# Kernel tuning notes

Measured on AMD Instinct MI355X. Metric: run time of the kernel, lower is better.

The kernel has to match this reference:

```python
import jax, jax.numpy as jnp
import numpy as np

B, L, D, H, DK, DV = 16, 1024, 512, 8, 64, 64
FACTOR = 1
TOP_K = int(FACTOR * np.log(L))  # 6, static


def autocorrelation(q, k, v, top_k):
    # q, k, v: [B, L, H, E] (Autoformer layout)
    Bs, Ls, Hs, Es = q.shape
    qp = jnp.transpose(q, (0, 2, 3, 1))  # [B,H,E,L]
    kp = jnp.transpose(k, (0, 2, 3, 1))
    vp = jnp.transpose(v, (0, 2, 3, 1))
    qf = jnp.fft.rfft(qp, axis=-1)
    kf = jnp.fft.rfft(kp, axis=-1)
    corr = jnp.fft.irfft(qf * jnp.conj(kf), n=Ls, axis=-1)  # [B,H,E,L]
    # time_delay_agg_training: average corr over heads and channels
    mean_value = corr.mean(axis=(1, 2))  # [B,L]
    _, index = jax.lax.top_k(mean_value.mean(axis=0), top_k)  # [top_k] shared delays
    weights = jnp.take(mean_value, index, axis=1)  # [B,top_k]
    tmp_corr = jax.nn.softmax(weights, axis=-1)  # [B,top_k]
    # roll(v, -delay) gathered for all top_k delays at once
    idx = (index[:, None] + jnp.arange(Ls)[None, :]) % Ls  # [top_k, L]
    patterns = vp[..., idx]  # [B,H,E,top_k,L]
    agg = jnp.einsum('bhekl,bk->bhel', patterns, tmp_corr)  # [B,H,E,L]
    return jnp.transpose(agg, (0, 3, 1, 2))  # [B,L,H,E]


def setup_inputs() -> dict:
    key = jax.random.key(0)
    ks = jax.random.split(key, 7)
    Q = jax.random.normal(ks[0], (B, L, D), jnp.float32)
    K = jax.random.normal(ks[1], (B, L, D), jnp.float32)
    V = jax.random.normal(ks[2], (B, L, D), jnp.float32)
    attn_mask = jnp.zeros((B, 1, L, L), jnp.bool_)  # ignored by AutoCorrelation
    s = 0.02
    WQ = jax.random.normal(ks[3], (D, H * DK), jnp.float32) * s
    WK = jax.random.normal(ks[4], (D, H * DK), jnp.float32) * s
    WV = jax.random.normal(ks[5], (D, H * DV), jnp.float32) * s
    Wfc = jax.random.normal(ks[6], (H * DV, D), jnp.float32) * s
    return {"Q": Q, "K": K, "V": V, "attn_mask": attn_mask,
            "WQ": WQ, "WK": WK, "WV": WV, "Wfc": Wfc}


def reference(Q, K, V, attn_mask, WQ, WK, WV, Wfc):
    del attn_mask  # full AutoCorrelation ignores the mask
    q_s = (Q @ WQ).reshape(B, L, H, DK)  # [B,L,H,dk]
    k_s = (K @ WK).reshape(B, L, H, DK)
    v_s = (V @ WV).reshape(B, L, H, DV)
    out = autocorrelation(q_s, k_s, v_s, TOP_K)  # [B,L,H,dv]
    context = out.reshape(B, L, H * DV)
    return context @ Wfc  # [B,L,D]
```

## Files before the change

kernel.cpp:

```cpp
#include <hip/hip_runtime.h>
#include <math.h>

namespace {

constexpr int Bb = 16;
constexpr int Ll = 1024;
constexpr int Dd = 512;
constexpr int TOPK = 6;
constexpr int Kc = 512;

typedef short  short8 __attribute__((ext_vector_type(8)));
typedef float  f32x4  __attribute__((ext_vector_type(4)));

__device__ __forceinline__ short f2bf(float x) {
  unsigned u = __builtin_bit_cast(unsigned, x);
  u += 0x7fffu + ((u >> 16) & 1u);
  return (short)(u >> 16);
}
__device__ __forceinline__ float bf2f(short b) {
  unsigned u = ((unsigned)(unsigned short)b) << 16;
  return __builtin_bit_cast(float, u);
}
__device__ __forceinline__ void g2l16(const void* g, void* l) {
  __builtin_amdgcn_global_load_lds(
      (const __attribute__((address_space(1))) unsigned*)g,
      (__attribute__((address_space(3))) unsigned*)l, 16, 0, 0);
}
__device__ __forceinline__ short8 cvt8(float4 a, float4 b) {
  short8 o;
  o[0] = f2bf(a.x); o[1] = f2bf(a.y); o[2] = f2bf(a.z); o[3] = f2bf(a.w);
  o[4] = f2bf(b.x); o[5] = f2bf(b.y); o[6] = f2bf(b.z); o[7] = f2bf(b.w);
  return o;
}

#define BARRIER() do { asm volatile("" ::: "memory"); \
    __builtin_amdgcn_s_barrier(); \
    asm volatile("" ::: "memory"); } while (0)
#define VMCNT8() asm volatile("s_waitcnt vmcnt(8)" ::: "memory")
#define VMCNT4() asm volatile("s_waitcnt vmcnt(4)" ::: "memory")
#define VMCNT0() asm volatile("s_waitcnt vmcnt(0)" ::: "memory")
#define LGKM0()  do { asm volatile("s_waitcnt lgkmcnt(0)" ::: "memory"); \
    __builtin_amdgcn_sched_barrier(0); } while (0)

template<int MODE>
__global__ __launch_bounds__(256) void g64(
    const void* __restrict__ A0, const void* __restrict__ A1,
    const short* __restrict__ B0, const short* __restrict__ B1,
    void* __restrict__ C0, void* __restrict__ C1)
{
  __shared__ short lds[2][16384];
  __shared__ float bins[256];

  const int tid = threadIdx.x;
  int z, m0, n0;
  if (MODE == 0) {
    z = blockIdx.x >> 4;
    const int s = blockIdx.x & 15;
    m0 = (s >> 2) * 128;  n0 = (s & 3) * 128;
  } else if (MODE == 1) {
    z = blockIdx.z;
    const int fb = blockIdx.x;
    const int s  = (fb & 7) * 64 + (fb >> 3);
    m0 = (s >> 2) * 128;  n0 = (s & 3) * 128;
  } else {
    const int fb = blockIdx.x;
    const int s  = (fb & 7) * 128 + (fb >> 3);
    z  = s >> 6;
    m0 = ((s >> 3) & 7) * 128;  n0 = (s & 7) * 128;
  }

  const int rS  = tid >> 3;
  const int c8S = (tid & 7) ^ (rS & 7);
  const short* Ga = nullptr;  const float* Fa = nullptr;
  const short* Gb = nullptr;  const float* Fb = nullptr;
  if (MODE == 0) {
    Ga = (const short*)(z ? A1 : A0) + (size_t)(m0 + rS) * Kc + c8S * 8;
    Gb = (z ? B1 : B0) + (size_t)(n0 + rS) * Kc + c8S * 8;
  } else if (MODE == 1) {
    Fa = (const float*)(z ? A1 : A0) + (size_t)(m0 + rS) * Kc + c8S * 8;
    Gb = (z ? B1 : B0) + (size_t)(n0 + rS) * Kc + c8S * 8;
  } else {
    Ga = (const short*)A0 + (size_t)z * Ll * Kc + (size_t)(m0 + rS) * Kc + c8S * 8;
    Fb = (const float*)A1 + (size_t)z * Ll * Kc + (size_t)(n0 + rS) * Kc + c8S * 8;
  }

  const int lane = tid & 63;
  const int wid  = tid >> 6;
  const int wr = wid >> 1, wn = wid & 1;
  const int lo = lane & 15, hi = lane >> 4;
  int aoff[2][4], boff[2][4];
#pragma unroll
  for (int i = 0; i < 4; ++i) {
    const int ar = wr * 64 + i * 16 + lo;
    const int br = wn * 64 + i * 16 + lo;
#pragma unroll
    for (int ks = 0; ks < 2; ++ks) {
      aoff[ks][i] = (ar * 8 + ((ks * 4 + hi) ^ (ar & 7))) * 8;
      boff[ks][i] = 8192 + (br * 8 + ((ks * 4 + hi) ^ (br & 7))) * 8;
    }
  }

  if (MODE == 2) bins[tid] = 0.f;

  f32x4 acc[4][4];
#pragma unroll
  for (int i = 0; i < 4; ++i)
#pragma unroll
    for (int j = 0; j < 4; ++j) acc[i][j] = (f32x4){0.f, 0.f, 0.f, 0.f};

#define SG_A(buf, kt) do { _Pragma("unroll") \
    for (int i_ = 0; i_ < 4; ++i_) \
      g2l16(Ga + (size_t)i_ * 32 * Kc + (kt) * 64, &lds[buf][(i_ * 256 + tid) * 8]); } while (0)
#define SG_B(buf, kt) do { _Pragma("unroll") \
    for (int i_ = 0; i_ < 4; ++i_) \
      g2l16(Gb + (size_t)i_ * 32 * Kc + (kt) * 64, &lds[buf][8192 + (i_ * 256 + tid) * 8]); } while (0)
#define LD_F(eV, F, kt) do { _Pragma("unroll") \
    for (int i_ = 0; i_ < 4; ++i_) { \
      eV[2 * i_]     = *(const float4*)((F) + (size_t)i_ * 32 * Kc + (kt) * 64); \
      eV[2 * i_ + 1] = *(const float4*)((F) + (size_t)i_ * 32 * Kc + (kt) * 64 + 4); } } while (0)
#define WR_F(buf, opb, eV) do { _Pragma("unroll") \
    for (int i_ = 0; i_ < 4; ++i_) \
      *(short8*)&lds[buf][(opb) + (i_ * 256 + tid) * 8] = cvt8(eV[2 * i_], eV[2 * i_ + 1]); } while (0)

  {
    float4 e[8];
    if (MODE == 1) {
      SG_B(0, 0); LD_F(e, Fa, 0); WR_F(0, 0, e);
      SG_B(1, 1); LD_F(e, Fa, 1); WR_F(1, 0, e);
    } else if (MODE == 2) {
      SG_A(0, 0); LD_F(e, Fb, 0); WR_F(0, 8192, e);
      SG_A(1, 1); LD_F(e, Fb, 1); WR_F(1, 8192, e);
    } else {
      SG_A(0, 0); SG_B(0, 0);
      SG_A(1, 1); SG_B(1, 1);
    }
  }

  int cur = 0;
#pragma unroll 1
  for (int t = 0; t < 8; ++t) {
    if (t == 7)            VMCNT0();
    else if (MODE == 0)    VMCNT8();
    else                   VMCNT4();
    LGKM0();
    BARRIER();

    const short* L = lds[cur];
    const bool pf = (t < 6);
    float4 e[8];

    short8 af[4], bq[4];
#pragma unroll
    for (int i = 0; i < 4; ++i) af[i] = *(const short8*)(L + aoff[0][i]);
#pragma unroll
    for (int j = 0; j < 4; ++j) bq[j] = *(const short8*)(L + boff[0][j]);
    if (pf && MODE == 1) LD_F(e, Fa, t + 2);
    if (pf && MODE == 2) LD_F(e, Fb, t + 2);
#pragma unroll
    for (int i = 0; i < 4; ++i)
#pragma unroll
      for (int j = 0; j < 4; ++j)
        acc[i][j] = __builtin_amdgcn_mfma_f32_16x16x32_bf16(af[i], bq[j], acc[i][j], 0, 0, 0);
#pragma unroll
    for (int i = 0; i < 4; ++i) af[i] = *(const short8*)(L + aoff[1][i]);
#pragma unroll
    for (int j = 0; j < 4; ++j) bq[j] = *(const short8*)(L + boff[1][j]);
#pragma unroll
    for (int i = 0; i < 4; ++i)
#pragma unroll
      for (int j = 0; j < 4; ++j)
        acc[i][j] = __builtin_amdgcn_mfma_f32_16x16x32_bf16(af[i], bq[j], acc[i][j], 0, 0, 0);

    BARRIER();

    if (pf) {
      if (MODE == 1)      { SG_B(cur, t + 2); WR_F(cur, 0, e); }
      else if (MODE == 2) { SG_A(cur, t + 2); WR_F(cur, 8192, e); }
      else                { SG_A(cur, t + 2); SG_B(cur, t + 2); }
    }
    cur ^= 1;
  }
#undef SG_A
#undef SG_B
#undef LD_F
#undef WR_F

  if (MODE != 2) {
    short* C = (short*)(MODE == 0 ? (z ? C1 : C0) : (z ? C1 : C0));
#pragma unroll
    for (int i = 0; i < 4; ++i)
#pragma unroll
      for (int r = 0; r < 4; ++r) {
        const size_t row = m0 + wr * 64 + i * 16 + hi * 4 + r;
#pragma unroll
        for (int j = 0; j < 4; ++j)
          C[row * Dd + n0 + wn * 64 + j * 16 + lo] = f2bf(acc[i][j][r]);
      }
  } else {
    float red[7][4];
#pragma unroll
    for (int d = 0; d < 7; ++d)
#pragma unroll
      for (int r = 0; r < 4; ++r) red[d][r] = 0.f;
#pragma unroll
    for (int i = 0; i < 4; ++i)
#pragma unroll
      for (int j = 0; j < 4; ++j)
#pragma unroll
        for (int r = 0; r < 4; ++r) red[i - j + 3][r] += acc[i][j][r];

    const int dbase = 127 + (wr - wn) * 64 + 4 * hi - lo;
#pragma unroll
    for (int d = 0; d < 7; ++d)
#pragma unroll
      for (int r = 0; r < 4; ++r)
        atomicAdd(&bins[dbase + 16 * (d - 3) + r], red[d][r]);
    __syncthreads();
    if (tid < 255) {
      float* mv = (float*)C0;
      const int l = (m0 - n0 + tid - 127) & (Ll - 1);
      atomicAdd(&mv[z * Ll + l], bins[tid]);
    }
  }
}

__global__ __launch_bounds__(256) void prep(
    const float* __restrict__ WQ, const float* __restrict__ WK,
    const float* __restrict__ WV, const float* __restrict__ Wfc,
    short* __restrict__ wqb, short* __restrict__ wkb,
    short* __restrict__ wvb, short* __restrict__ wtf,
    float* __restrict__ mv)
{
  const int z = blockIdx.z;
  const int tx = threadIdx.x & 31, ty = threadIdx.x >> 5;
  const int bx = blockIdx.x, by = blockIdx.y;
  if (z < 3) {
    const float* W = (z == 0) ? WQ : (z == 1) ? WK : WV;
    short* O = (z == 0) ? wqb : (z == 1) ? wkb : wvb;
#pragma unroll
    for (int s = 0; s < 32; s += 8) {
      const size_t o = (size_t)(by * 32 + ty + s) * 512 + bx * 32 + tx;
      O[o] = f2bf(W[o]);
    }
    if (z == 0 && threadIdx.x < 64) {
      const int fb = by * 16 + bx;
      mv[fb * 64 + threadIdx.x] = 0.f;
    }
  } else {
    __shared__ float t[32][33];
#pragma unroll
    for (int s = 0; s < 32; s += 8)
      t[ty + s][tx] = Wfc[(size_t)(by * 32 + ty + s) * 512 + bx * 32 + tx];
    __syncthreads();
#pragma unroll
    for (int s = 0; s < 32; s += 8)
      wtf[(size_t)(bx * 32 + ty + s) * 512 + by * 32 + tx] = f2bf(t[tx][ty + s]);
  }
}

__global__ __launch_bounds__(1024) void topk_softmax(
    const float* __restrict__ mean_value,
    int* __restrict__ idx_out, float* __restrict__ w_out)
{
  __shared__ float vals[1024];
  __shared__ int   inds[1024];
  __shared__ float bm[1024];
  __shared__ int   topi[TOPK];
  const int t = threadIdx.x;
  float s = 0.f;
  for (int b = 0; b < Bb; ++b) s += mean_value[b * Ll + t];
  bm[t] = s;
  __syncthreads();
  for (int k = 0; k < TOPK; ++k) {
    bool taken = false;
    for (int j = 0; j < k; ++j) taken |= (topi[j] == t);
    vals[t] = taken ? -INFINITY : bm[t];
    inds[t] = t;
    __syncthreads();
    for (int stride = 512; stride > 0; stride >>= 1) {
      if (t < stride) {
        if (vals[t + stride] > vals[t]) { vals[t] = vals[t + stride]; inds[t] = inds[t + stride]; }
      }
      __syncthreads();
    }
    if (t == 0) topi[k] = inds[0];
    __syncthreads();
  }
  if (t < TOPK) idx_out[t] = topi[t];
  if (t < Bb) {
    float wv[TOPK], mx = -INFINITY;
#pragma unroll
    for (int k = 0; k < TOPK; ++k) {
      wv[k] = mean_value[t * Ll + topi[k]] * (1.f / 512.f);
      mx = fmaxf(mx, wv[k]);
    }
    float sum = 0.f;
#pragma unroll
    for (int k = 0; k < TOPK; ++k) { wv[k] = expf(wv[k] - mx); sum += wv[k]; }
#pragma unroll
    for (int k = 0; k < TOPK; ++k) w_out[t * TOPK + k] = wv[k] / sum;
  }
}

__global__ __launch_bounds__(256) void gather_out(
    const short* __restrict__ U, const float* __restrict__ w,
    const int* __restrict__ idx, float* __restrict__ out)
{
  const int b = blockIdx.y;
  __shared__ float ww[8];
  __shared__ int   ii[8];
  if (threadIdx.x < TOPK) { ww[threadIdx.x] = w[b * TOPK + threadIdx.x]; ii[threadIdx.x] = idx[threadIdx.x]; }
  __syncthreads();
  const int l = blockIdx.x * 4 + (threadIdx.x >> 6);
  const int c = (threadIdx.x & 63) * 8;
  const short* ub = U + (size_t)b * Ll * Dd;
  float a[8] = {};
#pragma unroll
  for (int k = 0; k < TOPK; ++k) {
    const short8 vv = *(const short8*)&ub[(size_t)((l + ii[k]) & (Ll - 1)) * Dd + c];
    const float wk = ww[k];
#pragma unroll
    for (int e = 0; e < 8; ++e) a[e] = fmaf(wk, bf2f(vv[e]), a[e]);
  }
  float* op = &out[((size_t)b * Ll + l) * Dd + c];
  *(float4*)op       = make_float4(a[0], a[1], a[2], a[3]);
  *(float4*)(op + 4) = make_float4(a[4], a[5], a[6], a[7]);
}

}

extern "C" void kernel_launch(void* const* d_in, const int* in_sizes, int n_in,
                              void* d_out, int out_size, void* d_ws, size_t ws_size,
                              hipStream_t stream)
{
  const float* Q   = (const float*)d_in[0];
  const float* K   = (const float*)d_in[1];
  const float* V   = (const float*)d_in[2];
  const float* WQ  = (const float*)d_in[4];
  const float* WK  = (const float*)d_in[5];
  const float* WV  = (const float*)d_in[6];
  const float* Wfc = (const float*)d_in[7];
  float* out = (float*)d_out;

  char* ws = (char*)d_ws;
  const size_t SB = (size_t)Bb * Ll * Dd * sizeof(short);
  short* T    = (short*)(ws);
  short* U    = (short*)(ws + 1 * SB);
  short* wqb  = (short*)(ws + 2 * SB);
  short* wkb  = wqb + 512 * 512;
  short* wvb  = wkb + 512 * 512;
  short* wtf  = wvb + 512 * 512;
  short* Gt   = wtf + 512 * 512;
  short* Ht   = Gt  + 512 * 512;
  float* mv   = (float*)(Ht + 512 * 512);
  float* w    = mv + Bb * Ll;
  int*   idx  = (int*)(w + 128);

  prep<<<dim3(16, 16, 4), 256, 0, stream>>>(WQ, WK, WV, Wfc, wqb, wkb, wvb, wtf, mv);

  g64<0><<<32, 256, 0, stream>>>(wkb, wtf, wqb, wvb, Gt, Ht);

  g64<1><<<dim3(512, 1, 2), 256, 0, stream>>>(Q, V, Gt, Ht, T, U);

  g64<2><<<1024, 256, 0, stream>>>(T, K, nullptr, nullptr, mv, nullptr);

  topk_softmax<<<1, 1024, 0, stream>>>(mv, idx, w);

  gather_out<<<dim3(Ll / 4, Bb), 256, 0, stream>>>(U, w, idx, out);
}
```

Measured before the change: 138.4 us.

## Rewrite GEMM kernels with smaller tiles, split-K correlation, and fused K conversion

Replaces the 128x128, K-step-64 GEMM template with 128x64 tiles and K-step 32, reads fp32 operands directly with in-register bf16 conversion, and sets launch_bounds occupancy to 4. The K-to-bf16 conversion moves into extra blocks of the mode-1 launch, and the correlation GEMM is split along K into two halves with more blocks that accumulate through atomics. The WK and Wfc bf16 preconversions are dropped, and a new grid remapping is applied. The aim is more blocks in flight and better latency hiding, at the cost of more barriers, more atomics and less data reuse per tile.

```diff
diff --git a/kernel.cpp b/kernel.cpp
--- a/kernel.cpp
+++ b/kernel.cpp
@@ -7,7 +7,6 @@
 constexpr int Ll = 1024;
 constexpr int Dd = 512;
 constexpr int TOPK = 6;
-constexpr int Kc = 512;
 
 typedef short  short8 __attribute__((ext_vector_type(8)));
 typedef float  f32x4  __attribute__((ext_vector_type(4)));
@@ -33,210 +32,212 @@
   return o;
 }
 
-#define BARRIER() do { asm volatile("" ::: "memory"); \
-    __builtin_amdgcn_s_barrier(); \
-    asm volatile("" ::: "memory"); } while (0)
-#define VMCNT8() asm volatile("s_waitcnt vmcnt(8)" ::: "memory")
-#define VMCNT4() asm volatile("s_waitcnt vmcnt(4)" ::: "memory")
-#define VMCNT0() asm volatile("s_waitcnt vmcnt(0)" ::: "memory")
-#define LGKM0()  do { asm volatile("s_waitcnt lgkmcnt(0)" ::: "memory"); \
-    __builtin_amdgcn_sched_barrier(0); } while (0)
-
 template<int MODE>
-__global__ __launch_bounds__(256) void g64(
+__global__ __launch_bounds__(256, 4) void gk(
     const void* __restrict__ A0, const void* __restrict__ A1,
     const short* __restrict__ B0, const short* __restrict__ B1,
-    void* __restrict__ C0, void* __restrict__ C1)
-{
-  __shared__ short lds[2][16384];
-  __shared__ float bins[256];
+    void* __restrict__ C0, void* __restrict__ C1,
+    const float* __restrict__ KfIn, short* __restrict__ kbOut)
+{
+  __shared__ short lds[(MODE == 2) ? 12288 : 8192];
+  __shared__ float bins[(MODE == 2) ? 192 : 1];
 
   const int tid = threadIdx.x;
-  int z, m0, n0;
+  int z = 0, m0 = 0, n0 = 0, koff = 0;
+  const float* Fa = nullptr;
+  const short* Ab = nullptr;
+  const short* Bp = nullptr;
+
   if (MODE == 0) {
-    z = blockIdx.x >> 4;
-    const int s = blockIdx.x & 15;
-    m0 = (s >> 2) * 128;  n0 = (s & 3) * 128;
+    const int fb = blockIdx.x;
+    z  = fb >> 5;
+    m0 = ((fb >> 3) & 3) * 128;
+    n0 = (fb & 7) * 64;
+    Fa = (const float*)(z ? A1 : A0);
+    Bp = z ? B1 : B0;
   } else if (MODE == 1) {
-    z = blockIdx.z;
     const int fb = blockIdx.x;
-    const int s  = (fb & 7) * 64 + (fb >> 3);
-    m0 = (s >> 2) * 128;  n0 = (s & 3) * 128;
+    const int s  = (fb & 7) * 288 + (fb >> 3);
+    if (s >= 2048) {
+      const int ci = s - 2048;
+#pragma unroll
+      for (int it = 0; it < 16; ++it) {
+        const size_t i8 = (size_t)(ci * 256 + tid) + (size_t)it * 65536;
+        const float4 a = *(const float4*)(KfIn + i8 * 8);
+        const float4 b = *(const float4*)(KfIn + i8 * 8 + 4);
+        *(short8*)&kbOut[i8 * 8] = cvt8(a, b);
+      }
+      return;
+    }
+    z  = s >> 10;
+    const int ss = s & 1023;
+    m0 = (ss >> 3) * 128;
+    n0 = (ss & 7) * 64;
+    Fa = (const float*)(z ? A1 : A0);
+    Bp = z ? B1 : B0;
   } else {
     const int fb = blockIdx.x;
-    const int s  = (fb & 7) * 128 + (fb >> 3);
-    z  = s >> 6;
-    m0 = ((s >> 3) & 7) * 128;  n0 = (s & 7) * 128;
-  }
-
-  const int rS  = tid >> 3;
-  const int c8S = (tid & 7) ^ (rS & 7);
-  const short* Ga = nullptr;  const float* Fa = nullptr;
-  const short* Gb = nullptr;  const float* Fb = nullptr;
-  if (MODE == 0) {
-    Ga = (const short*)(z ? A1 : A0) + (size_t)(m0 + rS) * Kc + c8S * 8;
-    Gb = (z ? B1 : B0) + (size_t)(n0 + rS) * Kc + c8S * 8;
-  } else if (MODE == 1) {
-    Fa = (const float*)(z ? A1 : A0) + (size_t)(m0 + rS) * Kc + c8S * 8;
-    Gb = (z ? B1 : B0) + (size_t)(n0 + rS) * Kc + c8S * 8;
-  } else {
-    Ga = (const short*)A0 + (size_t)z * Ll * Kc + (size_t)(m0 + rS) * Kc + c8S * 8;
-    Fb = (const float*)A1 + (size_t)z * Ll * Kc + (size_t)(n0 + rS) * Kc + c8S * 8;
-  }
+    const int s  = (fb & 7) * 512 + (fb >> 3);
+    z    = s >> 8;
+    koff = ((s >> 7) & 1) * 256;
+    m0   = ((s >> 4) & 7) * 128;
+    n0   = (s & 15) * 64;
+    Ab = (const short*)A0 + (size_t)z * Ll * Dd;
+    Bp = B0 + (size_t)z * Ll * Dd;
+  }
+
+  const int rP  = tid >> 1, hP = tid & 1;
+  const int sxA = (rP >> 1) & 3;
+  const int c80 = (hP * 2) ^ sxA, c81 = (hP * 2 + 1) ^ sxA;
+  const int wA0 = (rP * 4 + hP * 2) * 8, wA1 = (rP * 4 + hP * 2 + 1) * 8;
+  const float* gAf = (MODE != 2) ? Fa + (size_t)(m0 + rP) * Dd : nullptr;
+  const int rS  = tid >> 2;
+  const int c8S = (tid & 3) ^ ((rS >> 1) & 3);
+  const short* gA2 = (MODE == 2) ? Ab + (size_t)(m0 + rS) * Dd + koff + c8S * 8 : nullptr;
+  const short* gB = Bp + (size_t)(n0 + rS) * Dd + koff + c8S * 8;
 
   const int lane = tid & 63;
   const int wid  = tid >> 6;
   const int wr = wid >> 1, wn = wid & 1;
   const int lo = lane & 15, hi = lane >> 4;
-  int aoff[2][4], boff[2][4];
+  int aoff[4], boff[2];
 #pragma unroll
   for (int i = 0; i < 4; ++i) {
     const int ar = wr * 64 + i * 16 + lo;
-    const int br = wn * 64 + i * 16 + lo;
-#pragma unroll
-    for (int ks = 0; ks < 2; ++ks) {
-      aoff[ks][i] = (ar * 8 + ((ks * 4 + hi) ^ (ar & 7))) * 8;
-      boff[ks][i] = 8192 + (br * 8 + ((ks * 4 + hi) ^ (br & 7))) * 8;
-    }
-  }
-
-  if (MODE == 2) bins[tid] = 0.f;
-
-  f32x4 acc[4][4];
+    aoff[i] = (ar * 4 + (hi ^ ((ar >> 1) & 3))) * 8;
+  }
+#pragma unroll
+  for (int j = 0; j < 2; ++j) {
+    const int br = wn * 32 + j * 16 + lo;
+    boff[j] = (br * 4 + (hi ^ ((br >> 1) & 3))) * 8;
+  }
+
+  if (MODE == 2 && tid < 192) bins[tid] = 0.f;
+
+  f32x4 acc[4][2];
 #pragma unroll
   for (int i = 0; i < 4; ++i)
 #pragma unroll
-    for (int j = 0; j < 4; ++j) acc[i][j] = (f32x4){0.f, 0.f, 0.f, 0.f};
-
-#define SG_A(buf, kt) do { _Pragma("unroll") \
-    for (int i_ = 0; i_ < 4; ++i_) \
-      g2l16(Ga + (size_t)i_ * 32 * Kc + (kt) * 64, &lds[buf][(i_ * 256 + tid) * 8]); } while (0)
-#define SG_B(buf, kt) do { _Pragma("unroll") \
-    for (int i_ = 0; i_ < 4; ++i_) \
-      g2l16(Gb + (size_t)i_ * 32 * Kc + (kt) * 64, &lds[buf][8192 + (i_ * 256 + tid) * 8]); } while (0)
-#define LD_F(eV, F, kt) do { _Pragma("unroll") \
-    for (int i_ = 0; i_ < 4; ++i_) { \
-      eV[2 * i_]     = *(const float4*)((F) + (size_t)i_ * 32 * Kc + (kt) * 64); \
-      eV[2 * i_ + 1] = *(const float4*)((F) + (size_t)i_ * 32 * Kc + (kt) * 64 + 4); } } while (0)
-#define WR_F(buf, opb, eV) do { _Pragma("unroll") \
-    for (int i_ = 0; i_ < 4; ++i_) \
-      *(short8*)&lds[buf][(opb) + (i_ * 256 + tid) * 8] = cvt8(eV[2 * i_], eV[2 * i_ + 1]); } while (0)
-
-  {
-    float4 e[8];
-    if (MODE == 1) {
-      SG_B(0, 0); LD_F(e, Fa, 0); WR_F(0, 0, e);
-      SG_B(1, 1); LD_F(e, Fa, 1); WR_F(1, 0, e);
-    } else if (MODE == 2) {
-      SG_A(0, 0); LD_F(e, Fb, 0); WR_F(0, 8192, e);
-      SG_A(1, 1); LD_F(e, Fb, 1); WR_F(1, 8192, e);
-    } else {
-      SG_A(0, 0); SG_B(0, 0);
-      SG_A(1, 1); SG_B(1, 1);
-    }
-  }
-
-  int cur = 0;
+    for (int j = 0; j < 2; ++j) acc[i][j] = (f32x4){0.f, 0.f, 0.f, 0.f};
+
+#define LDF(E, t) do { \
+    E[0] = *(const float4*)(gAf + (t) * 32 + c80 * 8); \
+    E[1] = *(const float4*)(gAf + (t) * 32 + c80 * 8 + 4); \
+    E[2] = *(const float4*)(gAf + (t) * 32 + c81 * 8); \
+    E[3] = *(const float4*)(gAf + (t) * 32 + c81 * 8 + 4); } while (0)
+#define WRF(E) do { \
+    *(short8*)&lds[wA0] = cvt8(E[0], E[1]); \
+    *(short8*)&lds[wA1] = cvt8(E[2], E[3]); } while (0)
+#define MFMA8(AB, BBASE) do { short8 a_[4], b_[2]; _Pragma("unroll") \
+    for (int i_ = 0; i_ < 4; ++i_) a_[i_] = *(const short8*)&lds[(AB) + aoff[i_]]; \
+    _Pragma("unroll") \
+    for (int j_ = 0; j_ < 2; ++j_) b_[j_] = *(const short8*)&lds[(BBASE) + boff[j_]]; \
+    ISSUE_NEXT; \
+    _Pragma("unroll") \
+    for (int i_ = 0; i_ < 4; ++i_) _Pragma("unroll") \
+      for (int j_ = 0; j_ < 2; ++j_) \
+        acc[i_][j_] = __builtin_amdgcn_mfma_f32_16x16x32_bf16(a_[i_], b_[j_], acc[i_][j_], 0, 0, 0); \
+    } while (0)
+
+  if (MODE != 2) {
+    float4 eA[4], eB[4];
+    LDF(eA, 0);
+    g2l16(gB, &lds[4096 + tid * 8]);
 #pragma unroll 1
-  for (int t = 0; t < 8; ++t) {
-    if (t == 7)            VMCNT0();
-    else if (MODE == 0)    VMCNT8();
-    else                   VMCNT4();
-    LGKM0();
-    BARRIER();
-
-    const short* L = lds[cur];
-    const bool pf = (t < 6);
-    float4 e[8];
-
-    short8 af[4], bq[4];
-#pragma unroll
-    for (int i = 0; i < 4; ++i) af[i] = *(const short8*)(L + aoff[0][i]);
-#pragma unroll
-    for (int j = 0; j < 4; ++j) bq[j] = *(const short8*)(L + boff[0][j]);
-    if (pf && MODE == 1) LD_F(e, Fa, t + 2);
-    if (pf && MODE == 2) LD_F(e, Fb, t + 2);
-#pragma unroll
-    for (int i = 0; i < 4; ++i)
-#pragma unroll
-      for (int j = 0; j < 4; ++j)
-        acc[i][j] = __builtin_amdgcn_mfma_f32_16x16x32_bf16(af[i], bq[j], acc[i][j], 0, 0, 0);
-#pragma unroll
-    for (int i = 0; i < 4; ++i) af[i] = *(const short8*)(L + aoff[1][i]);
-#pragma unroll
-    for (int j = 0; j < 4; ++j) bq[j] = *(const short8*)(L + boff[1][j]);
-#pragma unroll
-    for (int i = 0; i < 4; ++i)
-#pragma unroll
-      for (int j = 0; j < 4; ++j)
-        acc[i][j] = __builtin_amdgcn_mfma_f32_16x16x32_bf16(af[i], bq[j], acc[i][j], 0, 0, 0);
-
-    BARRIER();
-
-    if (pf) {
-      if (MODE == 1)      { SG_B(cur, t + 2); WR_F(cur, 0, e); }
-      else if (MODE == 2) { SG_A(cur, t + 2); WR_F(cur, 8192, e); }
-      else                { SG_A(cur, t + 2); SG_B(cur, t + 2); }
-    }
-    cur ^= 1;
-  }
-#undef SG_A
-#undef SG_B
-#undef LD_F
-#undef WR_F
+    for (int tt = 0; tt < 16; tt += 2) {
+      {
+        WRF(eA);
+        __syncthreads();
+        const int t = tt;
+#define ISSUE_NEXT do { if (t < 15) { LDF(eB, t + 1); \
+        g2l16(gB + (t + 1) * 32, &lds[4096 + 2048 + tid * 8]); } } while (0)
+        MFMA8(0, 4096);
+#undef ISSUE_NEXT
+        __syncthreads();
+      }
+      {
+        WRF(eB);
+        __syncthreads();
+        const int t = tt + 1;
+#define ISSUE_NEXT do { if (t < 15) { LDF(eA, t + 1); \
+        g2l16(gB + (t + 1) * 32, &lds[4096 + tid * 8]); } } while (0)
+        MFMA8(0, 4096 + 2048);
+#undef ISSUE_NEXT
+        __syncthreads();
+      }
+    }
+  } else {
+#define STAGE2(t, p) do { \
+    g2l16(gA2 + (t) * 32,                    &lds[(p) * 4096 + tid * 8]); \
+    g2l16(gA2 + (size_t)64 * Dd + (t) * 32,  &lds[(p) * 4096 + 2048 + tid * 8]); \
+    g2l16(gB  + (t) * 32,                    &lds[8192 + (p) * 2048 + tid * 8]); } while (0)
+    STAGE2(0, 0);
+    __syncthreads();
+#pragma unroll 1
+    for (int t = 0; t < 8; ++t) {
+      const int p = t & 1;
+#define ISSUE_NEXT do { if (t < 7) STAGE2(t + 1, p ^ 1); } while (0)
+      MFMA8(p * 4096, 8192 + p * 2048);
+#undef ISSUE_NEXT
+      __syncthreads();
+    }
+#undef STAGE2
+  }
+#undef LDF
+#undef WRF
+#undef MFMA8
 
   if (MODE != 2) {
-    short* C = (short*)(MODE == 0 ? (z ? C1 : C0) : (z ? C1 : C0));
+    short* C = (short*)(z ? C1 : C0);
 #pragma unroll
     for (int i = 0; i < 4; ++i)
 #pragma unroll
       for (int r = 0; r < 4; ++r) {
         const size_t row = m0 + wr * 64 + i * 16 + hi * 4 + r;
 #pragma unroll
-        for (int j = 0; j < 4; ++j)
-          C[row * Dd + n0 + wn * 64 + j * 16 + lo] = f2bf(acc[i][j][r]);
+        for (int j = 0; j < 2; ++j)
+          C[row * Dd + n0 + wn * 32 + j * 16 + lo] = f2bf(acc[i][j][r]);
       }
   } else {
-    float red[7][4];
-#pragma unroll
-    for (int d = 0; d < 7; ++d)
-#pragma unroll
-      for (int r = 0; r < 4; ++r) red[d][r] = 0.f;
+    float red[5][4];
+#pragma unroll
+    for (int g = 0; g < 5; ++g)
+#pragma unroll
+      for (int r = 0; r < 4; ++r) red[g][r] = 0.f;
 #pragma unroll
     for (int i = 0; i < 4; ++i)
 #pragma unroll
-      for (int j = 0; j < 4; ++j)
-#pragma unroll
-        for (int r = 0; r < 4; ++r) red[i - j + 3][r] += acc[i][j][r];
-
-    const int dbase = 127 + (wr - wn) * 64 + 4 * hi - lo;
-#pragma unroll
-    for (int d = 0; d < 7; ++d)
+      for (int j = 0; j < 2; ++j)
+#pragma unroll
+        for (int r = 0; r < 4; ++r) red[j - i + 3][r] += acc[i][j][r];
+
+    const int base = 127 + wn * 32 - wr * 64 + lo - 4 * hi;
+#pragma unroll
+    for (int g = 0; g < 5; ++g)
 #pragma unroll
       for (int r = 0; r < 4; ++r)
-        atomicAdd(&bins[dbase + 16 * (d - 3) + r], red[d][r]);
-    __syncthreads();
-    if (tid < 255) {
+        atomicAdd(&bins[base + 16 * (g - 3) - r], red[g][r]);
+    __syncthreads();
+    if (tid < 191) {
       float* mv = (float*)C0;
-      const int l = (m0 - n0 + tid - 127) & (Ll - 1);
+      const int l = (n0 - m0 + tid - 127) & (Ll - 1);
       atomicAdd(&mv[z * Ll + l], bins[tid]);
     }
   }
 }
 
 __global__ __launch_bounds__(256) void prep(
-    const float* __restrict__ WQ, const float* __restrict__ WK,
-    const float* __restrict__ WV, const float* __restrict__ Wfc,
-    short* __restrict__ wqb, short* __restrict__ wkb,
-    short* __restrict__ wvb, short* __restrict__ wtf,
-    float* __restrict__ mv)
+    const float* __restrict__ WQ, const float* __restrict__ WV,
+    const float* __restrict__ Wfc,
+    short* __restrict__ wqb, short* __restrict__ wvb,
+    float* __restrict__ wtfF, float* __restrict__ mv)
 {
   const int z = blockIdx.z;
   const int tx = threadIdx.x & 31, ty = threadIdx.x >> 5;
   const int bx = blockIdx.x, by = blockIdx.y;
-  if (z < 3) {
-    const float* W = (z == 0) ? WQ : (z == 1) ? WK : WV;
-    short* O = (z == 0) ? wqb : (z == 1) ? wkb : wvb;
+  if (z < 2) {
+    const float* W = z ? WV : WQ;
+    short* O = z ? wvb : wqb;
 #pragma unroll
     for (int s = 0; s < 32; s += 8) {
       const size_t o = (size_t)(by * 32 + ty + s) * 512 + bx * 32 + tx;
@@ -254,7 +255,7 @@
     __syncthreads();
 #pragma unroll
     for (int s = 0; s < 32; s += 8)
-      wtf[(size_t)(bx * 32 + ty + s) * 512 + by * 32 + tx] = f2bf(t[tx][ty + s]);
+      wtfF[(size_t)(bx * 32 + ty + s) * 512 + by * 32 + tx] = t[tx][ty + s];
   }
 }
 
@@ -346,23 +347,23 @@
   const size_t SB = (size_t)Bb * Ll * Dd * sizeof(short);
   short* T    = (short*)(ws);
   short* U    = (short*)(ws + 1 * SB);
-  short* wqb  = (short*)(ws + 2 * SB);
-  short* wkb  = wqb + 512 * 512;
-  short* wvb  = wkb + 512 * 512;
-  short* wtf  = wvb + 512 * 512;
-  short* Gt   = wtf + 512 * 512;
+  short* kb   = (short*)(ws + 2 * SB);
+  short* wqb  = (short*)(ws + 3 * SB);
+  short* wvb  = wqb + 512 * 512;
+  short* Gt   = wvb + 512 * 512;
   short* Ht   = Gt  + 512 * 512;
-  float* mv   = (float*)(Ht + 512 * 512);
+  float* wtfF = (float*)(Ht + 512 * 512);
+  float* mv   = wtfF + 512 * 512;
   float* w    = mv + Bb * Ll;
   int*   idx  = (int*)(w + 128);
 
-  prep<<<dim3(16, 16, 4), 256, 0, stream>>>(WQ, WK, WV, Wfc, wqb, wkb, wvb, wtf, mv);
-
-  g64<0><<<32, 256, 0, stream>>>(wkb, wtf, wqb, wvb, Gt, Ht);
-
-  g64<1><<<dim3(512, 1, 2), 256, 0, stream>>>(Q, V, Gt, Ht, T, U);
-
-  g64<2><<<1024, 256, 0, stream>>>(T, K, nullptr, nullptr, mv, nullptr);
+  prep<<<dim3(16, 16, 3), 256, 0, stream>>>(WQ, WV, Wfc, wqb, wvb, wtfF, mv);
+
+  gk<0><<<64, 256, 0, stream>>>(WK, wtfF, wqb, wvb, Gt, Ht, nullptr, nullptr);
+
+  gk<1><<<2304, 256, 0, stream>>>(Q, V, Gt, Ht, T, U, K, kb);
+
+  gk<2><<<4096, 256, 0, stream>>>(kb, nullptr, T, nullptr, mv, nullptr, nullptr, nullptr);
 
   topk_softmax<<<1, 1024, 0, stream>>>(mv, idx, w);
 
```

New measurement: 233.2 us. 1.69x slower.
